# Optimization experiments

Measured on AMD Instinct MI355X. Metric: run time of the kernel, lower is better.

## Reference

```python
import jax, jax.numpy as jnp
import numpy as np

N_NODES = 50000
N_EDGES = 1_600_000
Q_MULT = 8          # charges_irreps = 8x0e
NODE_MULT = 64      # node_feat_irreps = 64x0e + 64x1o
RBF = 8             # edge_feats_irreps num_irreps
HID = 64            # FullyConnectedNet hidden width
W_NUMEL = 2 * Q_MULT  # edge_tp weight_numel: two uvu paths (0e->0e, 0e x 1o->1o), u=8


def setup_inputs() -> dict:
    key = jax.random.key(0)
    k = jax.random.split(key, 14)
    f = lambda kk, sh: jax.random.normal(kk, sh, dtype=jnp.float32)
    return {
        "node_feats": f(k[0], (N_NODES, NODE_MULT * 4)),          # 64 scalars + 64 vectors(3)
        "charges_0": f(k[1], (N_NODES, Q_MULT)),                  # unused in forward
        "charges_induced": f(k[2], (N_NODES, Q_MULT)),
        "edge_feats": f(k[3], (N_EDGES, RBF)),
        "edge_attrs": f(k[4], (N_EDGES, 4)),                      # Y0 (1) + Y1 (3)
        "field_feats": f(k[5], (N_NODES, RBF)),                   # unused in forward
        "mlp_w1": f(k[6], (RBF, HID)),
        "mlp_w2": f(k[7], (HID, HID)),
        "mlp_w3": f(k[8], (HID, HID)),
        "mlp_w4": f(k[9], (HID, W_NUMEL)),
        "W0": f(k[10], (Q_MULT, NODE_MULT)),                      # node_tp path 0e x 0e -> 0e
        "W1": f(k[11], (Q_MULT, NODE_MULT)),                      # node_tp path 1o x 1o -> 0e
        "edge_index": jax.random.randint(k[12], (2, N_EDGES), 0, N_NODES, dtype=jnp.int32),
        "batch": jnp.zeros((N_NODES,), dtype=jnp.int32),
    }


def reference(node_feats, charges_0, charges_induced, edge_feats, edge_attrs,
              field_feats, mlp_w1, mlp_w2, mlp_w3, mlp_w4, W0, W1,
              edge_index, batch):
    sender, receiver = edge_index[0], edge_index[1]
    num_nodes = node_feats.shape[0]

    # e3nn FullyConnectedNet: variance-normalized linear layers + silu
    h = edge_feats
    for w in (mlp_w1, mlp_w2, mlp_w3):
        h = jax.nn.silu(h @ (w / np.sqrt(np.float32(w.shape[0]))))
    tp_w = h @ (mlp_w4 / np.sqrt(np.float32(mlp_w4.shape[0])))   # [E, 16]
    w0, w1 = tp_w[:, :Q_MULT], tp_w[:, Q_MULT:]                   # per-edge path weights

    # edge_tp (uvu, external weights): gather sender charges, weighted CG product
    q_s = charges_induced[sender]                                  # [E, 8]
    mid0 = (w0 * q_s) * edge_attrs[:, :1]                          # [E, 8]    0e
    mid1 = (w1 * q_s)[:, :, None] * edge_attrs[:, None, 1:4]       # [E, 8, 3] 1o

    # scatter-sum messages to receiver nodes
    sum0 = jax.ops.segment_sum(mid0, receiver, num_segments=num_nodes)
    sum1 = jax.ops.segment_sum(mid1.reshape(-1, Q_MULT * 3), receiver,
                               num_segments=num_nodes).reshape(-1, Q_MULT, 3)

    # node_tp: FullyConnectedTensorProduct(8x0e+8x1o, 64x0e+64x1o -> 1x0e)
    node0 = node_feats[:, :NODE_MULT]                              # [N, 64]
    node1 = node_feats[:, NODE_MULT:].reshape(-1, NODE_MULT, 3)    # [N, 64, 3]
    c = 1.0 / np.sqrt(np.float32(Q_MULT * NODE_MULT * 2))          # path normalization
    e0 = jnp.einsum('nu,nv,uv->n', sum0, node0, W0)
    e1 = jnp.einsum('nuk,nvk,uv->n', sum1, node1, W1) / np.sqrt(np.float32(3.0))  # w3j(1,1,0)
    return c * (e0 + e1)                                           # [N] per-node energy
```

## Files before the change

### kernel.cpp

```cpp
#include <hip/hip_runtime.h>
#include <hip/hip_bf16.h>

typedef short short8 __attribute__((ext_vector_type(8)));
typedef float f32x4 __attribute__((ext_vector_type(4)));

static __device__ __forceinline__ float bf2f(unsigned int b) { return __uint_as_float(b << 16); }
static __device__ __forceinline__ short fb2s(float x) {
    unsigned u = __float_as_uint(x);
    return (short)((u + 0x7FFFu + ((u >> 16) & 1u)) >> 16);
}
static __device__ __forceinline__ float silu(float x) {
    return x * __builtin_amdgcn_rcpf(1.0f + __expf(-x));
}
static __device__ __forceinline__ float load1(const void* p, long off, int isbf) {
    return isbf ? bf2f(((const unsigned short*)p)[off]) : ((const float*)p)[off];
}
static __device__ __forceinline__ void load4(const void* p, long off, int isbf, float* o) {
    if (isbf) {
        uint2 v = *(const uint2*)((const unsigned short*)p + off);
        o[0]=bf2f(v.x&0xffffu); o[1]=bf2f(v.x>>16);
        o[2]=bf2f(v.y&0xffffu); o[3]=bf2f(v.y>>16);
    } else {
        float4 v = *(const float4*)((const float*)p + off);
        o[0]=v.x; o[1]=v.y; o[2]=v.z; o[3]=v.w;
    }
}

__global__ void k_detect(const unsigned int* __restrict__ w, int* __restrict__ flag) {
    int lane = threadIdx.x & 63;
    unsigned int e = (w[lane] >> 7) & 0xFFu;
    unsigned long long m = __ballot(e >= 118u && e <= 132u);
    if (lane == 0) *flag = (__popcll(m) >= 32) ? 1 : 0;
}

__global__ void k_prepack(const void* __restrict__ w1, const void* __restrict__ w2,
                          const void* __restrict__ w3, const void* __restrict__ w4,
                          const int* __restrict__ flag, short* __restrict__ Bws) {
    int idx = blockIdx.x * 256 + threadIdx.x;
    if (idx >= 11264) return;
    const int isbf = *flag;
    int j = idx & 7, lane = (idx >> 3) & 63, tile = idx >> 9;
    int n16 = lane & 15, kq = lane >> 4;
    float v;
    if (tile < 4) {
        int k = kq * 8 + j, n = tile * 16 + n16;
        v = (k < 8) ? load1(w1, k * 64 + n, isbf) : 0.0f;
    } else if (tile < 12) {
        int t = (tile - 4) >> 1, kt = (tile - 4) & 1;
        int k = kt * 32 + kq * 8 + j, n = t * 16 + n16;
        v = load1(w2, k * 64 + n, isbf) * 0.125f;
    } else if (tile < 20) {
        int t = (tile - 12) >> 1, kt = (tile - 12) & 1;
        int k = kt * 32 + kq * 8 + j, n = t * 16 + n16;
        v = load1(w3, k * 64 + n, isbf) * 0.125f;
    } else {
        int kt = tile - 20;
        int k = kt * 32 + kq * 8 + j, n = n16;
        v = load1(w4, k * 16 + n, isbf) * 0.125f;
    }
    Bws[idx] = fb2s(v);
}

#define NB 32
__global__ __launch_bounds__(256) void k_nodeA(
    const void* __restrict__ nf, const void* __restrict__ W0, const void* __restrict__ W1,
    const int* __restrict__ flag, float* __restrict__ NA, int n_nodes) {
    __shared__ float Nd0[NB * 68];
    __shared__ float Nd1[3 * NB * 68];
    __shared__ float W0L[8 * 68];
    __shared__ float W1L[8 * 68];
    const int tid = threadIdx.x;
    const int isbf = *flag;
    const long n0 = (long)blockIdx.x * NB;

    for (int i = tid; i < 512; i += 256) {
        W0L[(i >> 6) * 68 + (i & 63)] = load1(W0, i, isbf);
        W1L[(i >> 6) * 68 + (i & 63)] = load1(W1, i, isbf);
    }
    if (isbf) {
        for (int i = tid; i < NB * 32; i += 256) {
            int node = i >> 5, c8 = (i & 31) * 8;
            long ng = n0 + node; if (ng > n_nodes - 1) ng = n_nodes - 1;
            uint4 v = *(const uint4*)((const unsigned short*)nf + ng * 256 + c8);
            float f[8];
            f[0]=bf2f(v.x&0xffffu); f[1]=bf2f(v.x>>16);
            f[2]=bf2f(v.y&0xffffu); f[3]=bf2f(v.y>>16);
            f[4]=bf2f(v.z&0xffffu); f[5]=bf2f(v.z>>16);
            f[6]=bf2f(v.w&0xffffu); f[7]=bf2f(v.w>>16);
            #pragma unroll
            for (int t = 0; t < 8; t++) {
                int col = c8 + t;
                if (col < 64) Nd0[node * 68 + col] = f[t];
                else {
                    int cc = col - 64, vv = cc / 3, kk = cc - vv * 3;
                    Nd1[(kk * NB + node) * 68 + vv] = f[t];
                }
            }
        }
    } else {
        for (int i = tid; i < NB * 64; i += 256) {
            int node = i >> 6, c4 = (i & 63) * 4;
            long ng = n0 + node; if (ng > n_nodes - 1) ng = n_nodes - 1;
            float4 v = *(const float4*)((const float*)nf + ng * 256 + c4);
            float f[4] = {v.x, v.y, v.z, v.w};
            #pragma unroll
            for (int t = 0; t < 4; t++) {
                int col = c4 + t;
                if (col < 64) Nd0[node * 68 + col] = f[t];
                else {
                    int cc = col - 64, vv = cc / 3, kk = cc - vv * 3;
                    Nd1[(kk * NB + node) * 68 + vv] = f[t];
                }
            }
        }
    }
    __syncthreads();

    const int wv = tid >> 6, lane = tid & 63;
    const int u = lane & 7, ln = lane >> 3;
    float sum[4] = {0.0f, 0.0f, 0.0f, 0.0f};

    if (wv == 0) {
        const float* w = &W0L[u * 68];
        for (int v0 = 0; v0 < 64; v0 += 4) {
            float4 w4 = *(const float4*)(w + v0);
            #pragma unroll
            for (int j = 0; j < 4; j++) {
                float4 nd = *(const float4*)&Nd0[(ln + 8 * j) * 68 + v0];
                sum[j] += w4.x * nd.x + w4.y * nd.y + w4.z * nd.z + w4.w * nd.w;
            }
        }
        #pragma unroll
        for (int j = 0; j < 4; j++) {
            long node = n0 + ln + 8 * j;
            if (node < n_nodes) NA[node * 32 + u] = sum[j] * 0.03125f;
        }
    } else {
        const int kk = wv - 1;
        const float* w = &W1L[u * 68];
        const float* nd1 = &Nd1[kk * NB * 68];
        for (int v0 = 0; v0 < 64; v0 += 4) {
            float4 w4 = *(const float4*)(w + v0);
            #pragma unroll
            for (int j = 0; j < 4; j++) {
                float4 nd = *(const float4*)&nd1[(ln + 8 * j) * 68 + v0];
                sum[j] += w4.x * nd.x + w4.y * nd.y + w4.z * nd.z + w4.w * nd.w;
            }
        }
        #pragma unroll
        for (int j = 0; j < 4; j++) {
            long node = n0 + ln + 8 * j;
            if (node < n_nodes) NA[node * 32 + 8 + u * 3 + kk] = sum[j] * 0.018042195912175804f;
        }
    }
}

__global__ __launch_bounds__(256) void k_edges_mfma(
    const void* __restrict__ ef, const void* __restrict__ ea, const void* __restrict__ qc,
    const int* __restrict__ eidx, const int* __restrict__ flag,
    const short* __restrict__ Bws, const float* __restrict__ NA,
    float* __restrict__ acc, int n_edges) {
    __shared__ short W[11264];
    __shared__ short Hs[4 * 2304];
    const int tid = threadIdx.x, lane = tid & 63, wv = tid >> 6;
    const int n16 = lane & 15, kq = lane >> 4;

    {
        const uint4* src = (const uint4*)Bws;
        uint4* dst = (uint4*)W;
        for (int i = tid; i < 1408; i += 256) dst[i] = src[i];
    }
    __syncthreads();

    const int isbf = *flag;
    const long E0 = (long)blockIdx.x * 128 + wv * 32;
    short* Hw = Hs + wv * 2304;

    short8 a1[2];
    #pragma unroll
    for (int mt = 0; mt < 2; mt++) {
        short8 a = {0,0,0,0,0,0,0,0};
        if (kq == 0) {
            long e = E0 + mt * 16 + n16;
            if (e > n_edges - 1) e = n_edges - 1;
            if (isbf) {
                a = *(const short8*)((const unsigned short*)ef + e * 8);
            } else {
                const float* pe = (const float*)ef + e * 8;
                float4 v0 = *(const float4*)pe, v1 = *(const float4*)(pe + 4);
                a[0]=fb2s(v0.x); a[1]=fb2s(v0.y); a[2]=fb2s(v0.z); a[3]=fb2s(v0.w);
                a[4]=fb2s(v1.x); a[5]=fb2s(v1.y); a[6]=fb2s(v1.z); a[7]=fb2s(v1.w);
            }
        }
        a1[mt] = a;
    }

    const f32x4 zero = {0.0f, 0.0f, 0.0f, 0.0f};

    {
        f32x4 c1[2][4];
        #pragma unroll
        for (int t = 0; t < 4; t++) {
            short8 b = *(const short8*)(W + t * 512 + lane * 8);
            #pragma unroll
            for (int mt = 0; mt < 2; mt++)
                c1[mt][t] = __builtin_amdgcn_mfma_f32_16x16x32_bf16(a1[mt], b, zero, 0, 0, 0);
        }
        #pragma unroll
        for (int mt = 0; mt < 2; mt++)
            #pragma unroll
            for (int t = 0; t < 4; t++)
                #pragma unroll
                for (int r = 0; r < 4; r++) {
                    float v = silu(c1[mt][t][r] * 0.35355339059327373f);
                    Hw[(mt * 16 + kq * 4 + r) * 72 + t * 16 + n16] = fb2s(v);
                }
    }

    #pragma unroll
    for (int L = 0; L < 2; L++) {
        const int base = (L == 0) ? 4 : 12;
        short8 a[2][2];
        #pragma unroll
        for (int mt = 0; mt < 2; mt++)
            #pragma unroll
            for (int kt = 0; kt < 2; kt++)
                a[mt][kt] = *(const short8*)(Hw + (mt * 16 + n16) * 72 + kq * 8 + kt * 32);
        f32x4 c2[2][4];
        #pragma unroll
        for (int mt = 0; mt < 2; mt++)
            #pragma unroll
            for (int t = 0; t < 4; t++) c2[mt][t] = zero;
        #pragma unroll
        for (int kt = 0; kt < 2; kt++)
            #pragma unroll
            for (int t = 0; t < 4; t++) {
                short8 b = *(const short8*)(W + (base + t * 2 + kt) * 512 + lane * 8);
                #pragma unroll
                for (int mt = 0; mt < 2; mt++)
                    c2[mt][t] = __builtin_amdgcn_mfma_f32_16x16x32_bf16(a[mt][kt], b, c2[mt][t], 0, 0, 0);
            }
        #pragma unroll
        for (int mt = 0; mt < 2; mt++)
            #pragma unroll
            for (int t = 0; t < 4; t++)
                #pragma unroll
                for (int r = 0; r < 4; r++) {
                    float v = silu(c2[mt][t][r]);
                    Hw[(mt * 16 + kq * 4 + r) * 72 + t * 16 + n16] = fb2s(v);
                }
    }

    float* TP = (float*)Hw;
    {
        short8 a[2][2];
        #pragma unroll
        for (int mt = 0; mt < 2; mt++)
            #pragma unroll
            for (int kt = 0; kt < 2; kt++)
                a[mt][kt] = *(const short8*)(Hw + (mt * 16 + n16) * 72 + kq * 8 + kt * 32);
        f32x4 c4[2] = {zero, zero};
        #pragma unroll
        for (int kt = 0; kt < 2; kt++) {
            short8 b = *(const short8*)(W + (20 + kt) * 512 + lane * 8);
            #pragma unroll
            for (int mt = 0; mt < 2; mt++)
                c4[mt] = __builtin_amdgcn_mfma_f32_16x16x32_bf16(a[mt][kt], b, c4[mt], 0, 0, 0);
        }
        #pragma unroll
        for (int mt = 0; mt < 2; mt++)
            #pragma unroll
            for (int r = 0; r < 4; r++)
                TP[(mt * 16 + kq * 4 + r) * 17 + n16] = c4[mt][r];
    }

    {
        const int el = lane >> 1, h = lane & 1;
        const long e = E0 + el;
        long ec = e;
        if (ec > n_edges - 1) ec = n_edges - 1;
        const int s = eidx[ec];
        const int r = eidx[(long)n_edges + ec];

        float tp0[4], tp1[4];
        #pragma unroll
        for (int i = 0; i < 4; i++) {
            tp0[i] = TP[el * 17 + h * 4 + i];
            tp1[i] = TP[el * 17 + 8 + h * 4 + i];
        }
        float q[4];
        load4(qc, (long)s * 8 + h * 4, isbf, q);
        float eav[4];
        load4(ea, ec * 4, isbf, eav);

        const float* nr = NA + (long)r * 32;
        float4 n0 = *(const float4*)(nr + h * 4);
        float t12[12];
        *(float4*)(t12 + 0) = *(const float4*)(nr + 8 + h * 12);
        *(float4*)(t12 + 4) = *(const float4*)(nr + 12 + h * 12);
        *(float4*)(t12 + 8) = *(const float4*)(nr + 16 + h * 12);

        float n0a[4] = {n0.x, n0.y, n0.z, n0.w};
        float p = 0.0f;
        #pragma unroll
        for (int i = 0; i < 4; i++) {
            float d = eav[1] * t12[i * 3] + eav[2] * t12[i * 3 + 1] + eav[3] * t12[i * 3 + 2];
            p += tp0[i] * q[i] * eav[0] * n0a[i] + tp1[i] * q[i] * d;
        }
        p += __shfl_xor(p, 1);
        if (h == 0 && e < n_edges) atomicAdd(&acc[r], p);
    }
}

__global__ void k_out(const float* __restrict__ acc, void* __restrict__ out,
                      const int* __restrict__ flag, int n) {
    int i = blockIdx.x * 256 + threadIdx.x;
    if (i >= n) return;
    if (*flag) ((__hip_bfloat16*)out)[i] = __float2bfloat16(acc[i]);
    else       ((float*)out)[i] = acc[i];
}

extern "C" void kernel_launch(void* const* d_in, const int* in_sizes, int n_in,
                              void* d_out, int out_size, void* d_ws, size_t ws_size,
                              hipStream_t stream) {
    const void* node_feats      = d_in[0];
    const void* charges_induced = d_in[2];
    const void* edge_feats      = d_in[3];
    const void* edge_attrs      = d_in[4];
    const void* mlp_w1          = d_in[6];
    const void* mlp_w2          = d_in[7];
    const void* mlp_w3          = d_in[8];
    const void* mlp_w4          = d_in[9];
    const void* W0              = d_in[10];
    const void* W1              = d_in[11];
    const int*  edge_index      = (const int*)d_in[12];

    const int n_nodes = in_sizes[0] / 256;
    const int n_edges = in_sizes[3] / 8;

    int*   flag = (int*)d_ws;
    short* Bws  = (short*)((char*)d_ws + 256);
    float* NA   = (float*)((char*)d_ws + 256 + 22528);
    float* acc  = NA + (size_t)n_nodes * 32;

    k_detect<<<1, 64, 0, stream>>>((const unsigned int*)node_feats, flag);
    hipMemsetAsync(acc, 0, (size_t)n_nodes * sizeof(float), stream);
    k_prepack<<<44, 256, 0, stream>>>(mlp_w1, mlp_w2, mlp_w3, mlp_w4, flag, Bws);
    k_nodeA<<<(n_nodes + NB - 1) / NB, 256, 0, stream>>>(node_feats, W0, W1, flag, NA, n_nodes);
    k_edges_mfma<<<(n_edges + 127) / 128, 256, 0, stream>>>(
        edge_feats, edge_attrs, charges_induced, edge_index, flag, Bws, NA, acc, n_edges);
    k_out<<<(n_nodes + 255) / 256, 256, 0, stream>>>(acc, d_out, flag, n_nodes);
}
```

Baseline: 340.9 us.

## Fuse detect/prepack/memset into node kernel and swizzle edge LDS layout

Removes the separate detect, prepack and memset launches by recomputing the bf16 detection in every kernel and folding the weight prepack and accumulator zeroing into the node kernel. In the edge kernel, the hidden-activation LDS layout is XOR-swizzled to cut bank conflicts, and bf16 rounding uses a cheaper round-half-up. The TP tile stride is padded to 20 so reads can be vectorised float4 loads. Costs: each block redoes a small detection load and ballot, and rounding differs slightly from round-to-nearest-even.

```diff
diff --git a/kernel.cpp b/kernel.cpp
--- a/kernel.cpp
+++ b/kernel.cpp
@@ -8,6 +8,9 @@
 static __device__ __forceinline__ short fb2s(float x) {
     unsigned u = __float_as_uint(x);
     return (short)((u + 0x7FFFu + ((u >> 16) & 1u)) >> 16);
+}
+static __device__ __forceinline__ short fb2s_fast(float x) {
+    return (short)((__float_as_uint(x) + 0x8000u) >> 16);
 }
 static __device__ __forceinline__ float silu(float x) {
     return x * __builtin_amdgcn_rcpf(1.0f + __expf(-x));
@@ -25,53 +28,56 @@
         o[0]=v.x; o[1]=v.y; o[2]=v.z; o[3]=v.w;
     }
 }
-
-__global__ void k_detect(const unsigned int* __restrict__ w, int* __restrict__ flag) {
+static __device__ __forceinline__ int detect_bf16(const void* nf) {
+    const unsigned int* w = (const unsigned int*)nf;
     int lane = threadIdx.x & 63;
     unsigned int e = (w[lane] >> 7) & 0xFFu;
     unsigned long long m = __ballot(e >= 118u && e <= 132u);
-    if (lane == 0) *flag = (__popcll(m) >= 32) ? 1 : 0;
-}
-
-__global__ void k_prepack(const void* __restrict__ w1, const void* __restrict__ w2,
-                          const void* __restrict__ w3, const void* __restrict__ w4,
-                          const int* __restrict__ flag, short* __restrict__ Bws) {
-    int idx = blockIdx.x * 256 + threadIdx.x;
-    if (idx >= 11264) return;
-    const int isbf = *flag;
-    int j = idx & 7, lane = (idx >> 3) & 63, tile = idx >> 9;
-    int n16 = lane & 15, kq = lane >> 4;
-    float v;
-    if (tile < 4) {
-        int k = kq * 8 + j, n = tile * 16 + n16;
-        v = (k < 8) ? load1(w1, k * 64 + n, isbf) : 0.0f;
-    } else if (tile < 12) {
-        int t = (tile - 4) >> 1, kt = (tile - 4) & 1;
-        int k = kt * 32 + kq * 8 + j, n = t * 16 + n16;
-        v = load1(w2, k * 64 + n, isbf) * 0.125f;
-    } else if (tile < 20) {
-        int t = (tile - 12) >> 1, kt = (tile - 12) & 1;
-        int k = kt * 32 + kq * 8 + j, n = t * 16 + n16;
-        v = load1(w3, k * 64 + n, isbf) * 0.125f;
-    } else {
-        int kt = tile - 20;
-        int k = kt * 32 + kq * 8 + j, n = n16;
-        v = load1(w4, k * 16 + n, isbf) * 0.125f;
-    }
-    Bws[idx] = fb2s(v);
+    return __popcll(m) >= 32 ? 1 : 0;
 }
 
 #define NB 32
-__global__ __launch_bounds__(256) void k_nodeA(
+__global__ __launch_bounds__(256) void k_node(
     const void* __restrict__ nf, const void* __restrict__ W0, const void* __restrict__ W1,
-    const int* __restrict__ flag, float* __restrict__ NA, int n_nodes) {
+    const void* __restrict__ w1, const void* __restrict__ w2,
+    const void* __restrict__ w3, const void* __restrict__ w4,
+    short* __restrict__ Bws, float* __restrict__ NA, float* __restrict__ acc, int n_nodes) {
     __shared__ float Nd0[NB * 68];
     __shared__ float Nd1[3 * NB * 68];
     __shared__ float W0L[8 * 68];
     __shared__ float W1L[8 * 68];
     const int tid = threadIdx.x;
-    const int isbf = *flag;
+    const int isbf = detect_bf16(nf);
     const long n0 = (long)blockIdx.x * NB;
+
+    if (blockIdx.x < 44) {
+        int idx = blockIdx.x * 256 + tid;
+        int j = idx & 7, lane = (idx >> 3) & 63, tile = idx >> 9;
+        int n16 = lane & 15, kq = lane >> 4;
+        float v;
+        if (tile < 4) {
+            int k = kq * 8 + j, n = tile * 16 + n16;
+            v = (k < 8) ? load1(w1, k * 64 + n, isbf) : 0.0f;
+        } else if (tile < 12) {
+            int t = (tile - 4) >> 1, kt = (tile - 4) & 1;
+            int k = kt * 32 + kq * 8 + j, n = t * 16 + n16;
+            v = load1(w2, k * 64 + n, isbf) * 0.125f;
+        } else if (tile < 20) {
+            int t = (tile - 12) >> 1, kt = (tile - 12) & 1;
+            int k = kt * 32 + kq * 8 + j, n = t * 16 + n16;
+            v = load1(w3, k * 64 + n, isbf) * 0.125f;
+        } else {
+            int kt = tile - 20;
+            int k = kt * 32 + kq * 8 + j, n = n16;
+            v = load1(w4, k * 16 + n, isbf) * 0.125f;
+        }
+        Bws[idx] = fb2s(v);
+    }
+    if (tid < NB) {
+        long n = n0 + tid;
+        if (n < n_nodes) acc[n] = 0.0f;
+    }
+    if (n0 >= n_nodes) return;
 
     for (int i = tid; i < 512; i += 256) {
         W0L[(i >> 6) * 68 + (i & 63)] = load1(W0, i, isbf);
@@ -157,13 +163,14 @@
 
 __global__ __launch_bounds__(256) void k_edges_mfma(
     const void* __restrict__ ef, const void* __restrict__ ea, const void* __restrict__ qc,
-    const int* __restrict__ eidx, const int* __restrict__ flag,
+    const int* __restrict__ eidx, const void* __restrict__ nf,
     const short* __restrict__ Bws, const float* __restrict__ NA,
     float* __restrict__ acc, int n_edges) {
     __shared__ short W[11264];
     __shared__ short Hs[4 * 2304];
     const int tid = threadIdx.x, lane = tid & 63, wv = tid >> 6;
     const int n16 = lane & 15, kq = lane >> 4;
+    const int isbf = detect_bf16(nf);
 
     {
         const uint4* src = (const uint4*)Bws;
@@ -172,9 +179,14 @@
     }
     __syncthreads();
 
-    const int isbf = *flag;
     const long E0 = (long)blockIdx.x * 128 + wv * 32;
     short* Hw = Hs + wv * 2304;
+
+    int woff[4];
+    #pragma unroll
+    for (int t = 0; t < 4; t++)
+        woff[t] = (((t * 2 + (n16 >> 3)) ^ (kq >> 1)) << 3) + (n16 & 7);
+    const int rbit = (n16 >> 3) & 1;
 
     short8 a1[2];
     #pragma unroll
@@ -213,7 +225,7 @@
                 #pragma unroll
                 for (int r = 0; r < 4; r++) {
                     float v = silu(c1[mt][t][r] * 0.35355339059327373f);
-                    Hw[(mt * 16 + kq * 4 + r) * 72 + t * 16 + n16] = fb2s(v);
+                    Hw[(mt * 16 + kq * 4 + r) * 72 + woff[t]] = fb2s_fast(v);
                 }
     }
 
@@ -225,7 +237,7 @@
         for (int mt = 0; mt < 2; mt++)
             #pragma unroll
             for (int kt = 0; kt < 2; kt++)
-                a[mt][kt] = *(const short8*)(Hw + (mt * 16 + n16) * 72 + kq * 8 + kt * 32);
+                a[mt][kt] = *(const short8*)(Hw + (mt * 16 + n16) * 72 + (((kt * 4 + kq) ^ rbit) << 3));
         f32x4 c2[2][4];
         #pragma unroll
         for (int mt = 0; mt < 2; mt++)
@@ -247,7 +259,7 @@
                 #pragma unroll
                 for (int r = 0; r < 4; r++) {
                     float v = silu(c2[mt][t][r]);
-                    Hw[(mt * 16 + kq * 4 + r) * 72 + t * 16 + n16] = fb2s(v);
+                    Hw[(mt * 16 + kq * 4 + r) * 72 + woff[t]] = fb2s_fast(v);
                 }
     }
 
@@ -258,7 +270,7 @@
         for (int mt = 0; mt < 2; mt++)
             #pragma unroll
             for (int kt = 0; kt < 2; kt++)
-                a[mt][kt] = *(const short8*)(Hw + (mt * 16 + n16) * 72 + kq * 8 + kt * 32);
+                a[mt][kt] = *(const short8*)(Hw + (mt * 16 + n16) * 72 + (((kt * 4 + kq) ^ rbit) << 3));
         f32x4 c4[2] = {zero, zero};
         #pragma unroll
         for (int kt = 0; kt < 2; kt++) {
@@ -271,7 +283,7 @@
         for (int mt = 0; mt < 2; mt++)
             #pragma unroll
             for (int r = 0; r < 4; r++)
-                TP[(mt * 16 + kq * 4 + r) * 17 + n16] = c4[mt][r];
+                TP[(mt * 16 + kq * 4 + r) * 20 + n16] = c4[mt][r];
     }
 
     {
@@ -282,12 +294,11 @@
         const int s = eidx[ec];
         const int r = eidx[(long)n_edges + ec];
 
-        float tp0[4], tp1[4];
-        #pragma unroll
-        for (int i = 0; i < 4; i++) {
-            tp0[i] = TP[el * 17 + h * 4 + i];
-            tp1[i] = TP[el * 17 + 8 + h * 4 + i];
-        }
+        float4 t0 = *(const float4*)(TP + el * 20 + h * 4);
+        float4 t1 = *(const float4*)(TP + el * 20 + 8 + h * 4);
+        float tp0[4] = {t0.x, t0.y, t0.z, t0.w};
+        float tp1[4] = {t1.x, t1.y, t1.z, t1.w};
+
         float q[4];
         load4(qc, (long)s * 8 + h * 4, isbf, q);
         float eav[4];
@@ -313,11 +324,12 @@
 }
 
 __global__ void k_out(const float* __restrict__ acc, void* __restrict__ out,
-                      const int* __restrict__ flag, int n) {
+                      const void* __restrict__ nf, int n) {
+    const int isbf = detect_bf16(nf);
     int i = blockIdx.x * 256 + threadIdx.x;
     if (i >= n) return;
-    if (*flag) ((__hip_bfloat16*)out)[i] = __float2bfloat16(acc[i]);
-    else       ((float*)out)[i] = acc[i];
+    if (isbf) ((__hip_bfloat16*)out)[i] = __float2bfloat16(acc[i]);
+    else      ((float*)out)[i] = acc[i];
 }
 
 extern "C" void kernel_launch(void* const* d_in, const int* in_sizes, int n_in,
@@ -338,16 +350,15 @@
     const int n_nodes = in_sizes[0] / 256;
     const int n_edges = in_sizes[3] / 8;
 
-    int*   flag = (int*)d_ws;
-    short* Bws  = (short*)((char*)d_ws + 256);
-    float* NA   = (float*)((char*)d_ws + 256 + 22528);
-    float* acc  = NA + (size_t)n_nodes * 32;
-
-    k_detect<<<1, 64, 0, stream>>>((const unsigned int*)node_feats, flag);
-    hipMemsetAsync(acc, 0, (size_t)n_nodes * sizeof(float), stream);
-    k_prepack<<<44, 256, 0, stream>>>(mlp_w1, mlp_w2, mlp_w3, mlp_w4, flag, Bws);
-    k_nodeA<<<(n_nodes + NB - 1) / NB, 256, 0, stream>>>(node_feats, W0, W1, flag, NA, n_nodes);
+    short* Bws = (short*)d_ws;
+    float* NA  = (float*)((char*)d_ws + 22528);
+    float* acc = NA + (size_t)n_nodes * 32;
+
+    int nblk = (n_nodes + NB - 1) / NB;
+    if (nblk < 44) nblk = 44;
+    k_node<<<nblk, 256, 0, stream>>>(node_feats, W0, W1,
+        mlp_w1, mlp_w2, mlp_w3, mlp_w4, Bws, NA, acc, n_nodes);
     k_edges_mfma<<<(n_edges + 127) / 128, 256, 0, stream>>>(
-        edge_feats, edge_attrs, charges_induced, edge_index, flag, Bws, NA, acc, n_edges);
-    k_out<<<(n_nodes + 255) / 256, 256, 0, stream>>>(acc, d_out, flag, n_nodes);
-}
+        edge_feats, edge_attrs, charges_induced, edge_index, node_feats, Bws, NA, acc, n_edges);
+    k_out<<<(n_nodes + 255) / 256, 256, 0, stream>>>(acc, d_out, node_feats, n_nodes);
+}
```

Result: no change. 337.3 us (-1.0%).
